# Performance work log

Hardware: AMD Instinct MI355X
Metric: run time of the kernel (lower is better)

The kernel has to match this reference:

```python
import jax, jax.numpy as jnp
import numpy as np
from jax import lax

IN_CH, OUT_CH, KS, GROUPS = 64, 64, 3, 8
FPG = IN_CH // GROUPS  # features per group = 8
PAD = KS // 2


def setup_inputs() -> dict:
    key = jax.random.key(0)
    k1, k2, k3 = jax.random.split(key, 3)
    x = jax.random.normal(k1, (8, IN_CH, 256, 256), dtype=jnp.float32)
    representation = jax.random.normal(k2, (8, 32), dtype=jnp.float32)
    # Linear(32, OUT_CH*KS*KS, bias=False) weight, torch layout (out_features, in_features)
    W = jax.random.normal(k3, (OUT_CH * KS * KS, 32), dtype=jnp.float32) * (1.0 / np.sqrt(32))
    return {"x": x, "representation": representation, "W": W}


def reference(x, representation, W):
    b = x.shape[0]
    # ReflectionPad2d
    xp = jnp.pad(x, ((0, 0), (0, 0), (PAD, PAD), (PAD, PAD)), mode="reflect")
    # compress_key: Linear (no bias) + LeakyReLU(0.1)
    k = jax.nn.leaky_relu(representation @ W.T, 0.1)  # [b, OUT_CH*KS*KS]
    kernel = k.reshape(b, OUT_CH, 1, KS, KS)
    # repeat_interleave on a size-1 dim == broadcast/tile
    kernel = jnp.broadcast_to(kernel, (b, OUT_CH, FPG, KS, KS))
    # per-sample grouped conv (equivalent to torch's batch-as-groups trick)
    def conv_one(xi, ki):
        # xi: [C,H,W], ki: [OUT_CH, FPG, KS, KS]
        out = lax.conv_general_dilated(
            xi[None], ki, window_strides=(1, 1), padding="VALID",
            dimension_numbers=("NCHW", "OIHW", "NCHW"),
            feature_group_count=GROUPS)
        return out[0]
    return jax.vmap(conv_one)(xp, kernel)  # [b, OUT_CH, H, W]
```

## Files before the change

### kernel.cpp

```cpp
#include <hip/hip_runtime.h>


#define LDSW 68
#define TH 32
#define TW 64

__device__ __forceinline__ int reflect1(int i, int n) {
  if (i < 0) i = -i;
  if (i >= n) i = 2 * n - 2 - i;
  return i;
}

__global__ __launch_bounds__(512) void dynconv_fused512(
    const float* __restrict__ x,
    const float* __restrict__ rep,
    const float* __restrict__ W,
    float* __restrict__ out) {
  const int tid = threadIdx.x;
  const int tx = blockIdx.x & 3;
  const int ty = (blockIdx.x >> 2) & 7;
  const int g  = (blockIdx.x >> 5) & 7;
  const int b  = blockIdx.x >> 8;

  __shared__ float s[(TH + 2) * LDSW];
  __shared__ float wl[96];

  if (tid < 72) {
    const int oc  = tid / 9;
    const int tap = tid - oc * 9;
    const int row = g * 72 + tid;
    const float* wr = W + (size_t)row * 32;
    const float* rb = rep + b * 32;
    float acc = 0.f;
#pragma unroll
    for (int j = 0; j < 32; ++j) acc += rb[j] * wr[j];
    wl[oc * 12 + tap] = (acc > 0.f) ? acc : 0.1f * acc;
  }

  const int gx0 = tx * TW, gy0 = ty * TH;
  const float* xg = x + ((size_t)(b * 64 + g * 8)) * 65536;
  const float4* xg4 = (const float4*)xg;

  for (int t = tid; t < 34 * 16; t += 512) {
    const int row = t >> 4, seg = t & 15;
    const int yy = reflect1(gy0 + row - 1, 256);
    const float4* p = xg4 + (size_t)yy * 64 + (gx0 >> 2) + seg;
    float4 v0 = p[0 * 16384], v1 = p[1 * 16384], v2 = p[2 * 16384], v3 = p[3 * 16384];
    float4 v4 = p[4 * 16384], v5 = p[5 * 16384], v6 = p[6 * 16384], v7 = p[7 * 16384];
    float4 a;
    a.x = ((v0.x + v1.x) + (v2.x + v3.x)) + ((v4.x + v5.x) + (v6.x + v7.x));
    a.y = ((v0.y + v1.y) + (v2.y + v3.y)) + ((v4.y + v5.y) + (v6.y + v7.y));
    a.z = ((v0.z + v1.z) + (v2.z + v3.z)) + ((v4.z + v5.z) + (v6.z + v7.z));
    a.w = ((v0.w + v1.w) + (v2.w + v3.w)) + ((v4.w + v5.w) + (v6.w + v7.w));
    *(float4*)&s[row * LDSW + seg * 4] = a;
  }
  if (tid < 68) {
    const int row = tid >> 1, side = tid & 1;
    const int scol = side ? 64 : 66;
    const int yy = reflect1(gy0 + row - 1, 256);
    const int xx = reflect1(gx0 + (side ? 64 : -1), 256);
    const float* p = xg + (size_t)yy * 256 + xx;
    float a = 0.f;
#pragma unroll
    for (int c = 0; c < 8; ++c) a += p[(size_t)c * 65536];
    s[row * LDSW + scol] = a;
  }
  __syncthreads();

  const int cs = (tid & 15) * 4;
  const int rr = tid >> 4;

  float win[3][6];
#pragma unroll
  for (int dy = 0; dy < 3; ++dy) {
    const float* row = &s[(rr + dy) * LDSW];
    float4 a = *(const float4*)&row[cs];
    float  r = row[cs + 4];
    float  l = row[(cs == 0) ? 66 : cs - 1];
    win[dy][0] = l;   win[dy][1] = a.x; win[dy][2] = a.y;
    win[dy][3] = a.z; win[dy][4] = a.w; win[dy][5] = r;
  }

  const int y = gy0 + rr;
  float* ob = out + (((size_t)(b * 64 + g * 8) * 256 + y) * 256 + gx0 + cs);

#pragma unroll
  for (int oc = 0; oc < 8; ++oc) {
    const float* w = &wl[oc * 12];
    const float w00 = w[0], w01 = w[1], w02 = w[2];
    const float w10 = w[3], w11 = w[4], w12 = w[5];
    const float w20 = w[6], w21 = w[7], w22 = w[8];
    float4 o;
    o.x = w00 * win[0][0] + w01 * win[0][1] + w02 * win[0][2]
        + w10 * win[1][0] + w11 * win[1][1] + w12 * win[1][2]
        + w20 * win[2][0] + w21 * win[2][1] + w22 * win[2][2];
    o.y = w00 * win[0][1] + w01 * win[0][2] + w02 * win[0][3]
        + w10 * win[1][1] + w11 * win[1][2] + w12 * win[1][3]
        + w20 * win[2][1] + w21 * win[2][2] + w22 * win[2][3];
    o.z = w00 * win[0][2] + w01 * win[0][3] + w02 * win[0][4]
        + w10 * win[1][2] + w11 * win[1][3] + w12 * win[1][4]
        + w20 * win[2][2] + w21 * win[2][3] + w22 * win[2][4];
    o.w = w00 * win[0][3] + w01 * win[0][4] + w02 * win[0][5]
        + w10 * win[1][3] + w11 * win[1][4] + w12 * win[1][5]
        + w20 * win[2][3] + w21 * win[2][4] + w22 * win[2][5];
    *(float4*)(ob + (size_t)oc * 65536) = o;
  }
}

extern "C" void kernel_launch(void* const* d_in, const int* in_sizes, int n_in,
                              void* d_out, int out_size, void* d_ws, size_t ws_size,
                              hipStream_t stream) {
  const float* x   = (const float*)d_in[0];
  const float* rep = (const float*)d_in[1];
  const float* W   = (const float*)d_in[2];
  float* out = (float*)d_out;
  hipLaunchKernelGGL(dynconv_fused512, dim3(2048), dim3(512), 0, stream,
                     x, rep, W, out);
}
```

Baseline: 246.7 us.

## Switch to full-width 8-row strip tiles to eliminate horizontal halo loads

Each block now covers an 8-row, full-width strip of one channel group instead of a 32x64 tile, with 256 threads each computing two output rows. Horizontal reflection is resolved inside shared memory, removing the separate scalar halo gather. The cost is a larger vertical halo fraction (10 input rows per 8 output rows), which increases redundant global reads of the 8-channel sums.

Result: faster. 241.1 us (-2.3%).

```diff
diff --git a/kernel.cpp b/kernel.cpp
--- a/kernel.cpp
+++ b/kernel.cpp
@@ -1,9 +1,8 @@
 #include <hip/hip_runtime.h>
 
 
-#define LDSW 68
-#define TH 32
-#define TW 64
+#define LROW 260
+#define TH 8
 
 __device__ __forceinline__ int reflect1(int i, int n) {
   if (i < 0) i = -i;
@@ -11,18 +10,17 @@
   return i;
 }
 
-__global__ __launch_bounds__(512) void dynconv_fused512(
+__global__ __launch_bounds__(256) void dynconv_rows(
     const float* __restrict__ x,
     const float* __restrict__ rep,
     const float* __restrict__ W,
     float* __restrict__ out) {
   const int tid = threadIdx.x;
-  const int tx = blockIdx.x & 3;
-  const int ty = (blockIdx.x >> 2) & 7;
+  const int ty = blockIdx.x & 31;
   const int g  = (blockIdx.x >> 5) & 7;
   const int b  = blockIdx.x >> 8;
 
-  __shared__ float s[(TH + 2) * LDSW];
+  __shared__ float s[(TH + 2) * LROW];
   __shared__ float wl[96];
 
   if (tid < 72) {
@@ -37,73 +35,70 @@
     wl[oc * 12 + tap] = (acc > 0.f) ? acc : 0.1f * acc;
   }
 
-  const int gx0 = tx * TW, gy0 = ty * TH;
+  const int gy0 = ty * TH;
   const float* xg = x + ((size_t)(b * 64 + g * 8)) * 65536;
   const float4* xg4 = (const float4*)xg;
 
-  for (int t = tid; t < 34 * 16; t += 512) {
-    const int row = t >> 4, seg = t & 15;
-    const int yy = reflect1(gy0 + row - 1, 256);
-    const float4* p = xg4 + (size_t)yy * 64 + (gx0 >> 2) + seg;
-    float4 v0 = p[0 * 16384], v1 = p[1 * 16384], v2 = p[2 * 16384], v3 = p[3 * 16384];
-    float4 v4 = p[4 * 16384], v5 = p[5 * 16384], v6 = p[6 * 16384], v7 = p[7 * 16384];
-    float4 a;
-    a.x = ((v0.x + v1.x) + (v2.x + v3.x)) + ((v4.x + v5.x) + (v6.x + v7.x));
-    a.y = ((v0.y + v1.y) + (v2.y + v3.y)) + ((v4.y + v5.y) + (v6.y + v7.y));
-    a.z = ((v0.z + v1.z) + (v2.z + v3.z)) + ((v4.z + v5.z) + (v6.z + v7.z));
-    a.w = ((v0.w + v1.w) + (v2.w + v3.w)) + ((v4.w + v5.w) + (v6.w + v7.w));
-    *(float4*)&s[row * LDSW + seg * 4] = a;
-  }
-  if (tid < 68) {
-    const int row = tid >> 1, side = tid & 1;
-    const int scol = side ? 64 : 66;
-    const int yy = reflect1(gy0 + row - 1, 256);
-    const int xx = reflect1(gx0 + (side ? 64 : -1), 256);
-    const float* p = xg + (size_t)yy * 256 + xx;
-    float a = 0.f;
 #pragma unroll
-    for (int c = 0; c < 8; ++c) a += p[(size_t)c * 65536];
-    s[row * LDSW + scol] = a;
+  for (int it = 0; it < 3; ++it) {
+    const int t = tid + it * 256;
+    if (it < 2 || t < 640) {
+      const int row = t >> 6, seg = t & 63;
+      const int yy = reflect1(gy0 + row - 1, 256);
+      const float4* p = xg4 + (size_t)yy * 64 + seg;
+      float4 v0 = p[0 * 16384], v1 = p[1 * 16384], v2 = p[2 * 16384], v3 = p[3 * 16384];
+      float4 v4 = p[4 * 16384], v5 = p[5 * 16384], v6 = p[6 * 16384], v7 = p[7 * 16384];
+      float4 a;
+      a.x = ((v0.x + v1.x) + (v2.x + v3.x)) + ((v4.x + v5.x) + (v6.x + v7.x));
+      a.y = ((v0.y + v1.y) + (v2.y + v3.y)) + ((v4.y + v5.y) + (v6.y + v7.y));
+      a.z = ((v0.z + v1.z) + (v2.z + v3.z)) + ((v4.z + v5.z) + (v6.z + v7.z));
+      a.w = ((v0.w + v1.w) + (v2.w + v3.w)) + ((v4.w + v5.w) + (v6.w + v7.w));
+      *(float4*)&s[row * LROW + seg * 4] = a;
+    }
   }
   __syncthreads();
 
-  const int cs = (tid & 15) * 4;
-  const int rr = tid >> 4;
-
-  float win[3][6];
-#pragma unroll
-  for (int dy = 0; dy < 3; ++dy) {
-    const float* row = &s[(rr + dy) * LDSW];
-    float4 a = *(const float4*)&row[cs];
-    float  r = row[cs + 4];
-    float  l = row[(cs == 0) ? 66 : cs - 1];
-    win[dy][0] = l;   win[dy][1] = a.x; win[dy][2] = a.y;
-    win[dy][3] = a.z; win[dy][4] = a.w; win[dy][5] = r;
-  }
-
-  const int y = gy0 + rr;
-  float* ob = out + (((size_t)(b * 64 + g * 8) * 256 + y) * 256 + gx0 + cs);
+  const int cs = (tid & 63) * 4;
+  const int r0 = tid >> 6;
 
 #pragma unroll
-  for (int oc = 0; oc < 8; ++oc) {
-    const float* w = &wl[oc * 12];
-    const float w00 = w[0], w01 = w[1], w02 = w[2];
-    const float w10 = w[3], w11 = w[4], w12 = w[5];
-    const float w20 = w[6], w21 = w[7], w22 = w[8];
-    float4 o;
-    o.x = w00 * win[0][0] + w01 * win[0][1] + w02 * win[0][2]
-        + w10 * win[1][0] + w11 * win[1][1] + w12 * win[1][2]
-        + w20 * win[2][0] + w21 * win[2][1] + w22 * win[2][2];
-    o.y = w00 * win[0][1] + w01 * win[0][2] + w02 * win[0][3]
-        + w10 * win[1][1] + w11 * win[1][2] + w12 * win[1][3]
-        + w20 * win[2][1] + w21 * win[2][2] + w22 * win[2][3];
-    o.z = w00 * win[0][2] + w01 * win[0][3] + w02 * win[0][4]
-        + w10 * win[1][2] + w11 * win[1][3] + w12 * win[1][4]
-        + w20 * win[2][2] + w21 * win[2][3] + w22 * win[2][4];
-    o.w = w00 * win[0][3] + w01 * win[0][4] + w02 * win[0][5]
-        + w10 * win[1][3] + w11 * win[1][4] + w12 * win[1][5]
-        + w20 * win[2][3] + w21 * win[2][4] + w22 * win[2][5];
-    *(float4*)(ob + (size_t)oc * 65536) = o;
+  for (int it = 0; it < 2; ++it) {
+    const int rr = r0 + it * 4;
+    float win[3][6];
+#pragma unroll
+    for (int dy = 0; dy < 3; ++dy) {
+      const float* row = &s[(rr + dy) * LROW];
+      float4 a = *(const float4*)&row[cs];
+      float  r = row[(cs == 252) ? 254 : cs + 4];
+      float  l = row[(cs == 0) ? 1 : cs - 1];
+      win[dy][0] = l;   win[dy][1] = a.x; win[dy][2] = a.y;
+      win[dy][3] = a.z; win[dy][4] = a.w; win[dy][5] = r;
+    }
+
+    const int y = gy0 + rr;
+    float* ob = out + (((size_t)(b * 64 + g * 8) * 256 + y) * 256 + cs);
+
+#pragma unroll
+    for (int oc = 0; oc < 8; ++oc) {
+      const float* w = &wl[oc * 12];
+      const float w00 = w[0], w01 = w[1], w02 = w[2];
+      const float w10 = w[3], w11 = w[4], w12 = w[5];
+      const float w20 = w[6], w21 = w[7], w22 = w[8];
+      float4 o;
+      o.x = w00 * win[0][0] + w01 * win[0][1] + w02 * win[0][2]
+          + w10 * win[1][0] + w11 * win[1][1] + w12 * win[1][2]
+          + w20 * win[2][0] + w21 * win[2][1] + w22 * win[2][2];
+      o.y = w00 * win[0][1] + w01 * win[0][2] + w02 * win[0][3]
+          + w10 * win[1][1] + w11 * win[1][2] + w12 * win[1][3]
+          + w20 * win[2][1] + w21 * win[2][2] + w22 * win[2][3];
+      o.z = w00 * win[0][2] + w01 * win[0][3] + w02 * win[0][4]
+          + w10 * win[1][2] + w11 * win[1][3] + w12 * win[1][4]
+          + w20 * win[2][2] + w21 * win[2][3] + w22 * win[2][4];
+      o.w = w00 * win[0][3] + w01 * win[0][4] + w02 * win[0][5]
+          + w10 * win[1][3] + w11 * win[1][4] + w12 * win[1][5]
+          + w20 * win[2][3] + w21 * win[2][4] + w22 * win[2][5];
+      *(float4*)(ob + (size_t)oc * 65536) = o;
+    }
   }
 }
 
@@ -114,6 +109,6 @@
   const float* rep = (const float*)d_in[1];
   const float* W   = (const float*)d_in[2];
   float* out = (float*)d_out;
-  hipLaunchKernelGGL(dynconv_fused512, dim3(2048), dim3(512), 0, stream,
+  hipLaunchKernelGGL(dynconv_rows, dim3(2048), dim3(256), 0, stream,
                      x, rep, W, out);
 }
```
